# Performance work log

Measured on AMD Instinct MI355X. Metric: run time of the kernel, lower is better.

The kernel has to match this reference:

```python
import jax, jax.numpy as jnp
import numpy as np

EMBED_DIM = 256
NUM_HEADS = 4
HEAD_DIM = EMBED_DIM // NUM_HEADS
SCALE = HEAD_DIM ** (-0.5)


def setup_inputs() -> dict:
    key = jax.random.key(0)
    kx, kq, kp, kb = jax.random.split(key, 4)
    B, N, C = 4, 4096, EMBED_DIM
    x = jax.random.normal(kx, (B, N, C), dtype=jnp.float32)
    # qkv: Linear(C, 3C, bias=False); torch stores weight as [out, in]
    w_qkv = jax.random.normal(kq, (3 * C, C), dtype=jnp.float32) * (C ** -0.5)
    w_proj = jax.random.normal(kp, (C, C), dtype=jnp.float32) * (C ** -0.5)
    b_proj = jax.random.normal(kb, (C,), dtype=jnp.float32) * 0.01
    return {"x": x, "w_qkv": w_qkv, "w_proj": w_proj, "b_proj": b_proj}


def reference(x, w_qkv, w_proj, b_proj):
    B, N, C = x.shape
    H, D = NUM_HEADS, HEAD_DIM
    # qkv projection: [B,N,3C] -> [3,B,H,N,D]
    qkv = (x @ w_qkv.T).reshape(B, N, 3, H, D).transpose(2, 0, 3, 1, 4)
    q, k, v = qkv[0], qkv[1], qkv[2]
    # materialized [B,H,N,N] scores (faithful to the original)
    attn = jnp.einsum("bhnd,bhmd->bhnm", q, k) * SCALE
    attn_probs = jax.nn.softmax(attn, axis=-1)
    out = jnp.einsum("bhnm,bhmd->bhnd", attn_probs, v)
    out = out.transpose(0, 2, 1, 3).reshape(B, N, C)
    return out @ w_proj.T + b_proj
```

## Files before the change

### kernel.cpp

```cpp
#include <hip/hip_runtime.h>
#include <hip/hip_bf16.h>

typedef __hip_bfloat16 bf16;
typedef _Float16 f16;
typedef __attribute__((ext_vector_type(8))) short bf16x8;
typedef __attribute__((ext_vector_type(8))) _Float16 f16x8;
typedef __attribute__((ext_vector_type(2))) _Float16 f16x2;
typedef __attribute__((ext_vector_type(4))) float f32x4;
typedef __attribute__((ext_vector_type(4))) unsigned int u32x4;
typedef __attribute__((ext_vector_type(2))) unsigned int u32x2;

#define B_ 4
#define N_ 4096
#define C_ 256
#define H_ 4
#define D_ 64
#define KLN 0.18033688011112042f

#if __has_builtin(__builtin_amdgcn_exp2f)
#define EXP2(x) __builtin_amdgcn_exp2f(x)
#else
#define EXP2(x) exp2f(x)
#endif
#if __has_builtin(__builtin_amdgcn_rcpf)
#define RCP(x) __builtin_amdgcn_rcpf(x)
#else
#define RCP(x) (1.0f / (x))
#endif

__device__ inline void load_lds16(const void* g, void* l) {
#if __has_builtin(__builtin_amdgcn_global_load_lds)
    __builtin_amdgcn_global_load_lds(
        (const __attribute__((address_space(1))) unsigned int*)g,
        (__attribute__((address_space(3))) unsigned int*)l, 16, 0, 0);
#else
    int ln = __lane_id();
    ((u32x4*)l)[ln] = *((const u32x4*)g);
#endif
}

__device__ inline unsigned int pk2(float a, float b) {
    unsigned int ua = __builtin_bit_cast(unsigned int, a) + 0x8000u;
    unsigned int ub = __builtin_bit_cast(unsigned int, b) + 0x8000u;
    return (ua >> 16) | (ub & 0xffff0000u);
}
__device__ inline unsigned int pkh2(float a, float b) {
#if __has_builtin(__builtin_amdgcn_cvt_pkrtz)
    return __builtin_bit_cast(unsigned int, __builtin_amdgcn_cvt_pkrtz(a, b));
#else
    f16x2 h = { (f16)a, (f16)b };
    return __builtin_bit_cast(unsigned int, h);
#endif
}
__device__ inline short f2s(float x) {
    return (short)__builtin_bit_cast(unsigned short, __float2bfloat16(x));
}
__device__ inline bf16x8 cvt8(const float* __restrict__ p) {
    f32x4 a = *reinterpret_cast<const f32x4*>(p);
    f32x4 b = *reinterpret_cast<const f32x4*>(p + 4);
    bf16x8 r = { f2s(a[0]), f2s(a[1]), f2s(a[2]), f2s(a[3]),
                 f2s(b[0]), f2s(b[1]), f2s(b[2]), f2s(b[3]) };
    return r;
}

__global__ __launch_bounds__(256) void cast_bf16(const float* __restrict__ x,
                                                 const float* __restrict__ wq,
                                                 const float* __restrict__ wp,
                                                 bf16* __restrict__ xb,
                                                 bf16* __restrict__ wqb,
                                                 bf16* __restrict__ wpb)
{
    int bid = blockIdx.x;
    const float* s; bf16* d; int base;
    if (bid < 2048)      { s = x;  d = xb;  base = bid * 2048; }
    else if (bid < 2144) { s = wq; d = wqb; base = (bid - 2048) * 2048; }
    else                 { s = wp; d = wpb; base = (bid - 2144) * 2048; }
    int i = base + threadIdx.x * 8;
    f32x4 a = *reinterpret_cast<const f32x4*>(s + i);
    f32x4 b = *reinterpret_cast<const f32x4*>(s + i + 4);
    u32x4 o;
    o.x = pk2(a[0], a[1]); o.y = pk2(a[2], a[3]);
    o.z = pk2(b[0], b[1]); o.w = pk2(b[2], b[3]);
    *reinterpret_cast<u32x4*>(d + i) = o;
}

__global__ __launch_bounds__(256, 2) void qkv_fast(const bf16* __restrict__ x,
                                                   const bf16* __restrict__ w,
                                                   bf16* __restrict__ qw,
                                                   bf16* __restrict__ kw,
                                                   f16* __restrict__ vtw)
{
    __shared__ short w_s[64][264];
    const int tid  = threadIdx.x;
    const int lane = tid & 63;
    const int wav  = tid >> 6;
    const int quad = lane >> 4;
    const int l16  = lane & 15;
    const int bid = (blockIdx.x & 7) * 192 + (blockIdx.x >> 3);
    const int mt = bid / 12, nb = bid % 12;
    const int m0 = mt * 128, n0 = nb * 64;

    {
        const int row = tid >> 2, cb = (tid & 3) * 64;
        const bf16* src = w + (size_t)(n0 + row) * C_ + cb;
#pragma unroll
        for (int i = 0; i < 8; ++i)
            *reinterpret_cast<bf16x8*>(&w_s[row][cb + i * 8]) =
                *reinterpret_cast<const bf16x8*>(src + i * 8);
    }
    __syncthreads();

#pragma unroll
    for (int half = 0; half < 2; ++half) {
        const int mh = m0 + half * 64;
        f32x4 acc[4] = {{0,0,0,0},{0,0,0,0},{0,0,0,0},{0,0,0,0}};
        const bf16* xrow = x + (size_t)(mh + wav * 16 + l16) * C_ + quad * 8;
        if (nb < 8) {
#pragma unroll
            for (int k0 = 0; k0 < C_; k0 += 32) {
                bf16x8 a = *reinterpret_cast<const bf16x8*>(xrow + k0);
#pragma unroll
                for (int nt = 0; nt < 4; ++nt) {
                    bf16x8 b = *reinterpret_cast<const bf16x8*>(&w_s[nt * 16 + l16][k0 + quad * 8]);
                    acc[nt] = __builtin_amdgcn_mfma_f32_16x16x32_bf16(b, a, acc[nt], 0, 0, 0);
                }
            }
        } else {
#pragma unroll
            for (int k0 = 0; k0 < C_; k0 += 32) {
                bf16x8 a = *reinterpret_cast<const bf16x8*>(xrow + k0);
#pragma unroll
                for (int nt = 0; nt < 4; ++nt) {
                    bf16x8 b = *reinterpret_cast<const bf16x8*>(&w_s[nt * 16 + l16][k0 + quad * 8]);
                    acc[nt] = __builtin_amdgcn_mfma_f32_16x16x32_bf16(a, b, acc[nt], 0, 0, 0);
                }
            }
        }

        const int bb = mh >> 12;
        const int nbase = (mh + wav * 16) & (N_ - 1);
        if (nb < 4) {
            bf16* dst = qw + (((size_t)bb * H_ + nb) * N_ + nbase + l16) * D_;
#pragma unroll
            for (int nt = 0; nt < 4; ++nt) {
                u32x2 wv = { pk2(acc[nt][0] * KLN, acc[nt][1] * KLN),
                             pk2(acc[nt][2] * KLN, acc[nt][3] * KLN) };
                *reinterpret_cast<u32x2*>(dst + nt * 16 + quad * 4) = wv;
            }
        } else if (nb < 8) {
            bf16* dst = kw + (((size_t)bb * H_ + (nb - 4)) * N_ + nbase + l16) * D_;
#pragma unroll
            for (int nt = 0; nt < 4; ++nt) {
                u32x2 wv = { pk2(acc[nt][0], acc[nt][1]),
                             pk2(acc[nt][2], acc[nt][3]) };
                *reinterpret_cast<u32x2*>(dst + nt * 16 + quad * 4) = wv;
            }
        } else {
            const int h = nb - 8;
#pragma unroll
            for (int nt = 0; nt < 4; ++nt) {
                int d = nt * 16 + l16;
                u32x2 wv;
                wv.x = pkh2(acc[nt][0], acc[nt][1]);
                wv.y = pkh2(acc[nt][2], acc[nt][3]);
                *reinterpret_cast<u32x2*>(
                    vtw + (((size_t)bb * H_ + h) * D_ + d) * N_ + nbase + quad * 4) = wv;
            }
        }
    }
}

__global__ __launch_bounds__(256) void qkv_cvt(const float* __restrict__ x,
                                               const float* __restrict__ w,
                                               bf16* __restrict__ qw,
                                               bf16* __restrict__ kw,
                                               f16* __restrict__ vtw)
{
    const int lane = threadIdx.x & 63;
    const int wav  = threadIdx.x >> 6;
    const int quad = lane >> 4;
    const int l16  = lane & 15;
    const int gw   = blockIdx.x * 4 + wav;
    const int m0   = (gw / 12) * 16;
    const int n0   = (gw % 12) * 64;

    f32x4 acc[4] = {{0,0,0,0},{0,0,0,0},{0,0,0,0},{0,0,0,0}};
    const float* xrow = x + (size_t)(m0 + l16) * C_ + quad * 8;
#pragma unroll
    for (int k0 = 0; k0 < C_; k0 += 32) {
        bf16x8 a = cvt8(xrow + k0);
#pragma unroll
        for (int nt = 0; nt < 4; ++nt) {
            bf16x8 b = cvt8(w + (size_t)(n0 + nt * 16 + l16) * C_ + k0 + quad * 8);
            acc[nt] = __builtin_amdgcn_mfma_f32_16x16x32_bf16(a, b, acc[nt], 0, 0, 0);
        }
    }
#pragma unroll
    for (int nt = 0; nt < 4; ++nt)
#pragma unroll
        for (int r = 0; r < 4; ++r) {
            int m  = m0 + quad * 4 + r;
            int o  = n0 + nt * 16 + l16;
            int bb = m >> 12;
            int n  = m & (N_ - 1);
            if (o < 256) {
                int h = o >> 6, d = o & 63;
                qw[(((size_t)bb * H_ + h) * N_ + n) * D_ + d] =
                    __float2bfloat16(acc[nt][r] * KLN);
            } else if (o < 512) {
                int oo = o - 256; int h = oo >> 6, d = oo & 63;
                kw[(((size_t)bb * H_ + h) * N_ + n) * D_ + d] =
                    __float2bfloat16(acc[nt][r]);
            } else {
                int oo = o - 512; int h = oo >> 6, d = oo & 63;
                vtw[(((size_t)bb * H_ + h) * D_ + d) * N_ + n] = (f16)acc[nt][r];
            }
        }
}

__global__ __launch_bounds__(256, 2) void attn(const bf16* __restrict__ q,
                                               const bf16* __restrict__ k,
                                               const f16* __restrict__ vt,
                                               bf16* __restrict__ o)
{
    __shared__ __align__(16) char smem[65536];
    short* k_s = reinterpret_cast<short*>(smem);
    f16*   v_s = reinterpret_cast<f16*>(smem + 32768);

    const int tid  = threadIdx.x;
    const int lane = tid & 63;
    const int wav  = tid >> 6;
    const int quad = lane >> 4;
    const int l16  = lane & 15;
    const int l8   = lane & 7;
    const int sub  = wav & 1;
    const int jh   = wav >> 1;

    const int wg = (blockIdx.x & 7) * 64 + (blockIdx.x >> 3);
    const int bh = wg >> 5;
    const int qt = wg & 31;
    const int bb = bh >> 2, h = bh & 3;

    const bf16* qp = q  + (size_t)bh * N_ * D_;
    const bf16* kp = k  + (size_t)bh * N_ * D_;
    const f16*  vp = vt + (size_t)bh * D_ * N_;

    const int qbase = qt * 128 + sub * 64;
    bf16x8 qb[4][2];
#pragma unroll
    for (int qg = 0; qg < 4; ++qg)
#pragma unroll
        for (int ks = 0; ks < 2; ++ks)
            qb[qg][ks] = *reinterpret_cast<const bf16x8*>(
                qp + (size_t)(qbase + qg * 16 + l16) * D_ + ks * 32 + quad * 8);

    const int ri = lane >> 3;
    const int ci = lane & 7;
    const int gc = ci ^ ri;
    int koff[4], voff[4], lds_r[4];
#pragma unroll
    for (int g = 0; g < 4; ++g) {
        const int rb  = sub * 32 + g * 8;
        const int rho = rb + ri;
        const int pr  = (rho & 32) | ((rho & 12) << 1) | ((rho & 16) >> 2) | (rho & 3);
        koff[g]  = pr * D_ + gc * 8;
        voff[g]  = rho * N_ + gc * 8;
        lds_r[g] = rb * 64;
    }

    f32x4 oacc[4][4];
    f32x4 lv[4];
#pragma unroll
    for (int qg = 0; qg < 4; ++qg) {
        lv[qg] = (f32x4){0, 0, 0, 0};
#pragma unroll
        for (int dt = 0; dt < 4; ++dt) oacc[qg][dt] = (f32x4){0, 0, 0, 0};
    }

    auto stage = [&](int buf, int t) {
        const int j0 = jh * 2048 + t * 64;
        short* kd = k_s + (size_t)(buf * 2 + jh) * 4096;
        f16*   vd = v_s + (size_t)(buf * 2 + jh) * 4096;
#pragma unroll
        for (int g = 0; g < 4; ++g) {
            load_lds16(kp + (size_t)j0 * D_ + koff[g], kd + lds_r[g]);
            load_lds16(vp + j0 + voff[g],              vd + lds_r[g]);
        }
    };

    stage(0, 0);
    __syncthreads();

    for (int t = 0; t < 32; ++t) {
        const int cur = t & 1;
        if (t < 31) stage(cur ^ 1, t + 1);

        const short* kt  = k_s + (size_t)(cur * 2 + jh) * 4096;
        const f16*   vtl = v_s + (size_t)(cur * 2 + jh) * 4096;

        f16x8 pb[4][2];
#pragma unroll
        for (int nt = 0; nt < 4; ++nt) {
            const int rb = (nt * 16 + l16) * 64;
            bf16x8 k0 = *reinterpret_cast<const bf16x8*>(kt + rb + ((quad    ) ^ l8) * 8);
            bf16x8 k1 = *reinterpret_cast<const bf16x8*>(kt + rb + ((4 + quad) ^ l8) * 8);
#pragma unroll
            for (int qg = 0; qg < 4; ++qg) {
                f32x4 sv = __builtin_amdgcn_mfma_f32_16x16x32_bf16(
                    k0, qb[qg][0], (f32x4){0.f, 0.f, 0.f, 0.f}, 0, 0, 0);
                sv = __builtin_amdgcn_mfma_f32_16x16x32_bf16(
                    k1, qb[qg][1], sv, 0, 0, 0);
                f32x4 pa = { EXP2(sv[0]), EXP2(sv[1]), EXP2(sv[2]), EXP2(sv[3]) };
                u32x2 pw = { pkh2(pa[0], pa[1]), pkh2(pa[2], pa[3]) };
                if (nt & 1)
                    *(reinterpret_cast<u32x2*>(&pb[qg][nt >> 1]) + 1) = pw;
                else
                    *(reinterpret_cast<u32x2*>(&pb[qg][nt >> 1]) + 0) = pw;
                lv[qg] += pa;
            }
        }

#pragma unroll
        for (int ks = 0; ks < 2; ++ks)
#pragma unroll
            for (int dt = 0; dt < 4; ++dt) {
                f16x8 va = *reinterpret_cast<const f16x8*>(
                    vtl + (dt * 16 + l16) * 64 + (((ks << 2) + quad) ^ l8) * 8);
#pragma unroll
                for (int qg = 0; qg < 4; ++qg)
                    oacc[qg][dt] = __builtin_amdgcn_mfma_f32_16x16x32_f16(va, pb[qg][ks], oacc[qg][dt], 0, 0, 0);
            }

        __syncthreads();
    }

    float lr[4];
#pragma unroll
    for (int qg = 0; qg < 4; ++qg) {
        float l = (lv[qg][0] + lv[qg][1]) + (lv[qg][2] + lv[qg][3]);
        l += __shfl_xor(l, 16);
        l += __shfl_xor(l, 32);
        lr[qg] = l;
    }

    float* mrg = reinterpret_cast<float*>(smem);
    const int slot = (sub * 64 + lane) * 69;
    if (jh == 1) {
#pragma unroll
        for (int qg = 0; qg < 4; ++qg) {
#pragma unroll
            for (int dt = 0; dt < 4; ++dt)
#pragma unroll
                for (int e = 0; e < 4; ++e)
                    mrg[slot + qg * 17 + dt * 4 + e] = oacc[qg][dt][e];
            mrg[slot + qg * 17 + 16] = lr[qg];
        }
    }
    __syncthreads();
    if (jh == 0) {
#pragma unroll
        for (int qg = 0; qg < 4; ++qg) {
            const float rl = RCP(lr[qg] + mrg[slot + qg * 17 + 16]);
            const size_t obase = ((size_t)bb * N_ + qbase + qg * 16 + l16) * C_ + h * D_;
#pragma unroll
            for (int dt = 0; dt < 4; ++dt) {
                float v0 = (oacc[qg][dt][0] + mrg[slot + qg * 17 + dt * 4 + 0]) * rl;
                float v1 = (oacc[qg][dt][1] + mrg[slot + qg * 17 + dt * 4 + 1]) * rl;
                float v2 = (oacc[qg][dt][2] + mrg[slot + qg * 17 + dt * 4 + 2]) * rl;
                float v3 = (oacc[qg][dt][3] + mrg[slot + qg * 17 + dt * 4 + 3]) * rl;
                u32x2 wv = { pk2(v0, v1), pk2(v2, v3) };
                *reinterpret_cast<u32x2*>(o + obase + dt * 16 + quad * 4) = wv;
            }
        }
    }
}

__global__ __launch_bounds__(256, 2) void out_proj_fast(const bf16* __restrict__ ov,
                                                        const bf16* __restrict__ w,
                                                        const float* __restrict__ bias,
                                                        float* __restrict__ out)
{
    __shared__ short w_s[64][264];
    const int tid  = threadIdx.x;
    const int lane = tid & 63;
    const int wav  = tid >> 6;
    const int quad = lane >> 4;
    const int l16  = lane & 15;
    const int bid = (blockIdx.x & 7) * 64 + (blockIdx.x >> 3);
    const int m0 = (bid >> 2) * 128;
    const int n0 = (bid & 3) * 64;

    {
        const int row = tid >> 2, cb = (tid & 3) * 64;
        const bf16* src = w + (size_t)(n0 + row) * C_ + cb;
#pragma unroll
        for (int i = 0; i < 8; ++i)
            *reinterpret_cast<bf16x8*>(&w_s[row][cb + i * 8]) =
                *reinterpret_cast<const bf16x8*>(src + i * 8);
    }
    __syncthreads();

#pragma unroll
    for (int half = 0; half < 2; ++half) {
        const int mh = m0 + half * 64;
        f32x4 acc[4] = {{0,0,0,0},{0,0,0,0},{0,0,0,0},{0,0,0,0}};
        const bf16* orow = ov + (size_t)(mh + wav * 16 + l16) * C_ + quad * 8;
#pragma unroll
        for (int k0 = 0; k0 < C_; k0 += 32) {
            bf16x8 a = *reinterpret_cast<const bf16x8*>(orow + k0);
#pragma unroll
            for (int nt = 0; nt < 4; ++nt) {
                bf16x8 b = *reinterpret_cast<const bf16x8*>(&w_s[nt * 16 + l16][k0 + quad * 8]);
                acc[nt] = __builtin_amdgcn_mfma_f32_16x16x32_bf16(b, a, acc[nt], 0, 0, 0);
            }
        }
        const int m = mh + wav * 16 + l16;
#pragma unroll
        for (int nt = 0; nt < 4; ++nt) {
            const int oc0 = n0 + nt * 16 + quad * 4;
            f32x4 bv = *reinterpret_cast<const f32x4*>(bias + oc0);
            f32x4 ovv = acc[nt] + bv;
            *reinterpret_cast<f32x4*>(out + (size_t)m * C_ + oc0) = ovv;
        }
    }
}

__global__ __launch_bounds__(256) void out_proj_cvt(const bf16* __restrict__ ov,
                                                    const float* __restrict__ w,
                                                    const float* __restrict__ bias,
                                                    float* __restrict__ out)
{
    const int lane = threadIdx.x & 63;
    const int wav  = threadIdx.x >> 6;
    const int quad = lane >> 4;
    const int l16  = lane & 15;
    const int gw   = blockIdx.x * 4 + wav;
    const int m0   = (gw >> 2) * 16;
    const int n0   = (gw & 3) * 64;

    f32x4 acc[4] = {{0,0,0,0},{0,0,0,0},{0,0,0,0},{0,0,0,0}};
    const bf16* orow = ov + (size_t)(m0 + l16) * C_ + quad * 8;
#pragma unroll
    for (int k0 = 0; k0 < C_; k0 += 32) {
        bf16x8 a = *reinterpret_cast<const bf16x8*>(orow + k0);
#pragma unroll
        for (int nt = 0; nt < 4; ++nt) {
            bf16x8 b = cvt8(w + (size_t)(n0 + nt * 16 + l16) * C_ + k0 + quad * 8);
            acc[nt] = __builtin_amdgcn_mfma_f32_16x16x32_bf16(a, b, acc[nt], 0, 0, 0);
        }
    }
#pragma unroll
    for (int nt = 0; nt < 4; ++nt)
#pragma unroll
        for (int r = 0; r < 4; ++r) {
            int m  = m0 + quad * 4 + r;
            int oc = n0 + nt * 16 + l16;
            out[(size_t)m * C_ + oc] = acc[nt][r] + bias[oc];
        }
}

extern "C" void kernel_launch(void* const* d_in, const int* in_sizes, int n_in,
                              void* d_out, int out_size, void* d_ws, size_t ws_size,
                              hipStream_t stream) {
    const float* x      = (const float*)d_in[0];
    const float* w_qkv  = (const float*)d_in[1];
    const float* w_proj = (const float*)d_in[2];
    const float* b_proj = (const float*)d_in[3];
    float* out = (float*)d_out;

    const size_t qkv_elems = (size_t)B_ * H_ * N_ * D_;
    bf16* q_ws  = (bf16*)d_ws;
    bf16* k_ws  = q_ws  + qkv_elems;
    f16*  vt_ws = (f16*)(k_ws + qkv_elems);
    bf16* o_ws  = (bf16*)(vt_ws + qkv_elems);
    bf16* x_bf  = o_ws  + qkv_elems;
    bf16* wq_bf = x_bf  + (size_t)B_ * N_ * C_;
    bf16* wp_bf = wq_bf + (size_t)3 * C_ * C_;

    const size_t need = ((size_t)4 * qkv_elems + (size_t)B_ * N_ * C_
                         + (size_t)3 * C_ * C_ + (size_t)C_ * C_) * 2;

    if (ws_size >= need) {
        cast_bf16    <<<2176, 256, 0, stream>>>(x, w_qkv, w_proj, x_bf, wq_bf, wp_bf);
        qkv_fast     <<<1536, 256, 0, stream>>>(x_bf, wq_bf, q_ws, k_ws, vt_ws);
        attn         <<< 512, 256, 0, stream>>>(q_ws, k_ws, vt_ws, o_ws);
        out_proj_fast<<< 512, 256, 0, stream>>>(o_ws, wp_bf, b_proj, out);
    } else {
        qkv_cvt      <<<3072, 256, 0, stream>>>(x, w_qkv, q_ws, k_ws, vt_ws);
        attn         <<< 512, 256, 0, stream>>>(q_ws, k_ws, vt_ws, o_ws);
        out_proj_cvt <<<1024, 256, 0, stream>>>(o_ws, w_proj, b_proj, out);
    }
}
```

Baseline: 174.8 us.

## Fuse fp32->bf16 casts into GEMMs and load K/V directly to registers in attention

Removes the separate cast kernel by converting fp32 x and weights to bf16 inside the QKV and output projection kernels. The attention kernel stops staging K/V tiles through LDS with async global-to-LDS copies and a per-tile barrier; each wave now prefetches its K and V fragments straight from global memory into registers for the next tile. This saves a kernel launch and an extra round trip of x through memory, and removes the per-iteration barriers. The cost is more register pressure, and K/V loads are no longer shared across waves, so global/L2 traffic goes up.

```diff
diff --git a/kernel.cpp b/kernel.cpp
--- a/kernel.cpp
+++ b/kernel.cpp
@@ -28,17 +28,6 @@
 #define RCP(x) (1.0f / (x))
 #endif
 
-__device__ inline void load_lds16(const void* g, void* l) {
-#if __has_builtin(__builtin_amdgcn_global_load_lds)
-    __builtin_amdgcn_global_load_lds(
-        (const __attribute__((address_space(1))) unsigned int*)g,
-        (__attribute__((address_space(3))) unsigned int*)l, 16, 0, 0);
-#else
-    int ln = __lane_id();
-    ((u32x4*)l)[ln] = *((const u32x4*)g);
-#endif
-}
-
 __device__ inline unsigned int pk2(float a, float b) {
     unsigned int ua = __builtin_bit_cast(unsigned int, a) + 0x8000u;
     unsigned int ub = __builtin_bit_cast(unsigned int, b) + 0x8000u;
@@ -52,40 +41,16 @@
     return __builtin_bit_cast(unsigned int, h);
 #endif
 }
-__device__ inline short f2s(float x) {
-    return (short)__builtin_bit_cast(unsigned short, __float2bfloat16(x));
-}
-__device__ inline bf16x8 cvt8(const float* __restrict__ p) {
+__device__ inline bf16x8 cvt8pk(const float* __restrict__ p) {
     f32x4 a = *reinterpret_cast<const f32x4*>(p);
     f32x4 b = *reinterpret_cast<const f32x4*>(p + 4);
-    bf16x8 r = { f2s(a[0]), f2s(a[1]), f2s(a[2]), f2s(a[3]),
-                 f2s(b[0]), f2s(b[1]), f2s(b[2]), f2s(b[3]) };
-    return r;
-}
-
-__global__ __launch_bounds__(256) void cast_bf16(const float* __restrict__ x,
-                                                 const float* __restrict__ wq,
-                                                 const float* __restrict__ wp,
-                                                 bf16* __restrict__ xb,
-                                                 bf16* __restrict__ wqb,
-                                                 bf16* __restrict__ wpb)
-{
-    int bid = blockIdx.x;
-    const float* s; bf16* d; int base;
-    if (bid < 2048)      { s = x;  d = xb;  base = bid * 2048; }
-    else if (bid < 2144) { s = wq; d = wqb; base = (bid - 2048) * 2048; }
-    else                 { s = wp; d = wpb; base = (bid - 2144) * 2048; }
-    int i = base + threadIdx.x * 8;
-    f32x4 a = *reinterpret_cast<const f32x4*>(s + i);
-    f32x4 b = *reinterpret_cast<const f32x4*>(s + i + 4);
-    u32x4 o;
-    o.x = pk2(a[0], a[1]); o.y = pk2(a[2], a[3]);
-    o.z = pk2(b[0], b[1]); o.w = pk2(b[2], b[3]);
-    *reinterpret_cast<u32x4*>(d + i) = o;
-}
-
-__global__ __launch_bounds__(256, 2) void qkv_fast(const bf16* __restrict__ x,
-                                                   const bf16* __restrict__ w,
+    u32x4 o = { pk2(a[0], a[1]), pk2(a[2], a[3]),
+                pk2(b[0], b[1]), pk2(b[2], b[3]) };
+    return __builtin_bit_cast(bf16x8, o);
+}
+
+__global__ __launch_bounds__(256, 2) void qkv_fast(const float* __restrict__ x,
+                                                   const float* __restrict__ w,
                                                    bf16* __restrict__ qw,
                                                    bf16* __restrict__ kw,
                                                    f16* __restrict__ vtw)
@@ -102,11 +67,15 @@
 
     {
         const int row = tid >> 2, cb = (tid & 3) * 64;
-        const bf16* src = w + (size_t)(n0 + row) * C_ + cb;
-#pragma unroll
-        for (int i = 0; i < 8; ++i)
-            *reinterpret_cast<bf16x8*>(&w_s[row][cb + i * 8]) =
-                *reinterpret_cast<const bf16x8*>(src + i * 8);
+        const float* src = w + (size_t)(n0 + row) * C_ + cb;
+#pragma unroll
+        for (int i = 0; i < 8; ++i) {
+            f32x4 a = *reinterpret_cast<const f32x4*>(src + i * 8);
+            f32x4 b = *reinterpret_cast<const f32x4*>(src + i * 8 + 4);
+            u32x4 ov = { pk2(a[0], a[1]), pk2(a[2], a[3]),
+                         pk2(b[0], b[1]), pk2(b[2], b[3]) };
+            *reinterpret_cast<u32x4*>(&w_s[row][cb + i * 8]) = ov;
+        }
     }
     __syncthreads();
 
@@ -114,11 +83,11 @@
     for (int half = 0; half < 2; ++half) {
         const int mh = m0 + half * 64;
         f32x4 acc[4] = {{0,0,0,0},{0,0,0,0},{0,0,0,0},{0,0,0,0}};
-        const bf16* xrow = x + (size_t)(mh + wav * 16 + l16) * C_ + quad * 8;
+        const float* xrow = x + (size_t)(mh + wav * 16 + l16) * C_ + quad * 8;
         if (nb < 8) {
 #pragma unroll
             for (int k0 = 0; k0 < C_; k0 += 32) {
-                bf16x8 a = *reinterpret_cast<const bf16x8*>(xrow + k0);
+                bf16x8 a = cvt8pk(xrow + k0);
 #pragma unroll
                 for (int nt = 0; nt < 4; ++nt) {
                     bf16x8 b = *reinterpret_cast<const bf16x8*>(&w_s[nt * 16 + l16][k0 + quad * 8]);
@@ -128,7 +97,7 @@
         } else {
 #pragma unroll
             for (int k0 = 0; k0 < C_; k0 += 32) {
-                bf16x8 a = *reinterpret_cast<const bf16x8*>(xrow + k0);
+                bf16x8 a = cvt8pk(xrow + k0);
 #pragma unroll
                 for (int nt = 0; nt < 4; ++nt) {
                     bf16x8 b = *reinterpret_cast<const bf16x8*>(&w_s[nt * 16 + l16][k0 + quad * 8]);
@@ -170,69 +139,18 @@
     }
 }
 
-__global__ __launch_bounds__(256) void qkv_cvt(const float* __restrict__ x,
-                                               const float* __restrict__ w,
-                                               bf16* __restrict__ qw,
-                                               bf16* __restrict__ kw,
-                                               f16* __restrict__ vtw)
-{
-    const int lane = threadIdx.x & 63;
-    const int wav  = threadIdx.x >> 6;
-    const int quad = lane >> 4;
-    const int l16  = lane & 15;
-    const int gw   = blockIdx.x * 4 + wav;
-    const int m0   = (gw / 12) * 16;
-    const int n0   = (gw % 12) * 64;
-
-    f32x4 acc[4] = {{0,0,0,0},{0,0,0,0},{0,0,0,0},{0,0,0,0}};
-    const float* xrow = x + (size_t)(m0 + l16) * C_ + quad * 8;
-#pragma unroll
-    for (int k0 = 0; k0 < C_; k0 += 32) {
-        bf16x8 a = cvt8(xrow + k0);
-#pragma unroll
-        for (int nt = 0; nt < 4; ++nt) {
-            bf16x8 b = cvt8(w + (size_t)(n0 + nt * 16 + l16) * C_ + k0 + quad * 8);
-            acc[nt] = __builtin_amdgcn_mfma_f32_16x16x32_bf16(a, b, acc[nt], 0, 0, 0);
-        }
-    }
-#pragma unroll
-    for (int nt = 0; nt < 4; ++nt)
-#pragma unroll
-        for (int r = 0; r < 4; ++r) {
-            int m  = m0 + quad * 4 + r;
-            int o  = n0 + nt * 16 + l16;
-            int bb = m >> 12;
-            int n  = m & (N_ - 1);
-            if (o < 256) {
-                int h = o >> 6, d = o & 63;
-                qw[(((size_t)bb * H_ + h) * N_ + n) * D_ + d] =
-                    __float2bfloat16(acc[nt][r] * KLN);
-            } else if (o < 512) {
-                int oo = o - 256; int h = oo >> 6, d = oo & 63;
-                kw[(((size_t)bb * H_ + h) * N_ + n) * D_ + d] =
-                    __float2bfloat16(acc[nt][r]);
-            } else {
-                int oo = o - 512; int h = oo >> 6, d = oo & 63;
-                vtw[(((size_t)bb * H_ + h) * D_ + d) * N_ + n] = (f16)acc[nt][r];
-            }
-        }
-}
-
 __global__ __launch_bounds__(256, 2) void attn(const bf16* __restrict__ q,
                                                const bf16* __restrict__ k,
                                                const f16* __restrict__ vt,
                                                bf16* __restrict__ o)
 {
-    __shared__ __align__(16) char smem[65536];
-    short* k_s = reinterpret_cast<short*>(smem);
-    f16*   v_s = reinterpret_cast<f16*>(smem + 32768);
+    __shared__ float mrg[8832];
 
     const int tid  = threadIdx.x;
     const int lane = tid & 63;
     const int wav  = tid >> 6;
     const int quad = lane >> 4;
     const int l16  = lane & 15;
-    const int l8   = lane & 7;
     const int sub  = wav & 1;
     const int jh   = wav >> 1;
 
@@ -254,18 +172,11 @@
             qb[qg][ks] = *reinterpret_cast<const bf16x8*>(
                 qp + (size_t)(qbase + qg * 16 + l16) * D_ + ks * 32 + quad * 8);
 
-    const int ri = lane >> 3;
-    const int ci = lane & 7;
-    const int gc = ci ^ ri;
-    int koff[4], voff[4], lds_r[4];
-#pragma unroll
-    for (int g = 0; g < 4; ++g) {
-        const int rb  = sub * 32 + g * 8;
-        const int rho = rb + ri;
-        const int pr  = (rho & 32) | ((rho & 12) << 1) | ((rho & 16) >> 2) | (rho & 3);
-        koff[g]  = pr * D_ + gc * 8;
-        voff[g]  = rho * N_ + gc * 8;
-        lds_r[g] = rb * 64;
+    int krow[4];
+#pragma unroll
+    for (int nt = 0; nt < 4; ++nt) {
+        const int rho = nt * 16 + l16;
+        krow[nt] = (rho & 32) | ((rho & 12) << 1) | ((rho & 16) >> 2) | (rho & 3);
     }
 
     f32x4 oacc[4][4];
@@ -277,33 +188,31 @@
         for (int dt = 0; dt < 4; ++dt) oacc[qg][dt] = (f32x4){0, 0, 0, 0};
     }
 
-    auto stage = [&](int buf, int t) {
-        const int j0 = jh * 2048 + t * 64;
-        short* kd = k_s + (size_t)(buf * 2 + jh) * 4096;
-        f16*   vd = v_s + (size_t)(buf * 2 + jh) * 4096;
-#pragma unroll
-        for (int g = 0; g < 4; ++g) {
-            load_lds16(kp + (size_t)j0 * D_ + koff[g], kd + lds_r[g]);
-            load_lds16(vp + j0 + voff[g],              vd + lds_r[g]);
-        }
-    };
-
-    stage(0, 0);
-    __syncthreads();
+    const int j00 = jh * 2048;
+
+    bf16x8 kf[4][2];
+    f16x8  vf[2][4];
+#pragma unroll
+    for (int nt = 0; nt < 4; ++nt)
+#pragma unroll
+        for (int ks = 0; ks < 2; ++ks)
+            kf[nt][ks] = *reinterpret_cast<const bf16x8*>(
+                kp + (size_t)(j00 + krow[nt]) * D_ + ks * 32 + quad * 8);
+#pragma unroll
+    for (int ks = 0; ks < 2; ++ks)
+#pragma unroll
+        for (int dt = 0; dt < 4; ++dt)
+            vf[ks][dt] = *reinterpret_cast<const f16x8*>(
+                vp + (size_t)(dt * 16 + l16) * N_ + j00 + (ks * 4 + quad) * 8);
 
     for (int t = 0; t < 32; ++t) {
-        const int cur = t & 1;
-        if (t < 31) stage(cur ^ 1, t + 1);
-
-        const short* kt  = k_s + (size_t)(cur * 2 + jh) * 4096;
-        const f16*   vtl = v_s + (size_t)(cur * 2 + jh) * 4096;
+        const int jn = j00 + (t + 1) * 64;
 
         f16x8 pb[4][2];
 #pragma unroll
         for (int nt = 0; nt < 4; ++nt) {
-            const int rb = (nt * 16 + l16) * 64;
-            bf16x8 k0 = *reinterpret_cast<const bf16x8*>(kt + rb + ((quad    ) ^ l8) * 8);
-            bf16x8 k1 = *reinterpret_cast<const bf16x8*>(kt + rb + ((4 + quad) ^ l8) * 8);
+            const bf16x8 k0 = kf[nt][0];
+            const bf16x8 k1 = kf[nt][1];
 #pragma unroll
             for (int qg = 0; qg < 4; ++qg) {
                 f32x4 sv = __builtin_amdgcn_mfma_f32_16x16x32_bf16(
@@ -318,20 +227,27 @@
                     *(reinterpret_cast<u32x2*>(&pb[qg][nt >> 1]) + 0) = pw;
                 lv[qg] += pa;
             }
+            if (t < 31) {
+                kf[nt][0] = *reinterpret_cast<const bf16x8*>(
+                    kp + (size_t)(jn + krow[nt]) * D_ + quad * 8);
+                kf[nt][1] = *reinterpret_cast<const bf16x8*>(
+                    kp + (size_t)(jn + krow[nt]) * D_ + 32 + quad * 8);
+            }
         }
 
 #pragma unroll
         for (int ks = 0; ks < 2; ++ks)
 #pragma unroll
             for (int dt = 0; dt < 4; ++dt) {
-                f16x8 va = *reinterpret_cast<const f16x8*>(
-                    vtl + (dt * 16 + l16) * 64 + (((ks << 2) + quad) ^ l8) * 8);
+                const f16x8 va = vf[ks][dt];
 #pragma unroll
                 for (int qg = 0; qg < 4; ++qg)
-                    oacc[qg][dt] = __builtin_amdgcn_mfma_f32_16x16x32_f16(va, pb[qg][ks], oacc[qg][dt], 0, 0, 0);
-            }
-
-        __syncthreads();
+                    oacc[qg][dt] = __builtin_amdgcn_mfma_f32_16x16x32_f16(
+                        va, pb[qg][ks], oacc[qg][dt], 0, 0, 0);
+                if (t < 31)
+                    vf[ks][dt] = *reinterpret_cast<const f16x8*>(
+                        vp + (size_t)(dt * 16 + l16) * N_ + jn + (ks * 4 + quad) * 8);
+            }
     }
 
     float lr[4];
@@ -343,8 +259,8 @@
         lr[qg] = l;
     }
 
-    float* mrg = reinterpret_cast<float*>(smem);
     const int slot = (sub * 64 + lane) * 69;
+    __syncthreads();
     if (jh == 1) {
 #pragma unroll
         for (int qg = 0; qg < 4; ++qg) {
@@ -376,7 +292,7 @@
 }
 
 __global__ __launch_bounds__(256, 2) void out_proj_fast(const bf16* __restrict__ ov,
-                                                        const bf16* __restrict__ w,
+                                                        const float* __restrict__ w,
                                                         const float* __restrict__ bias,
                                                         float* __restrict__ out)
 {
@@ -392,11 +308,15 @@
 
     {
         const int row = tid >> 2, cb = (tid & 3) * 64;
-        const bf16* src = w + (size_t)(n0 + row) * C_ + cb;
-#pragma unroll
-        for (int i = 0; i < 8; ++i)
-            *reinterpret_cast<bf16x8*>(&w_s[row][cb + i * 8]) =
-                *reinterpret_cast<const bf16x8*>(src + i * 8);
+        const float* src = w + (size_t)(n0 + row) * C_ + cb;
+#pragma unroll
+        for (int i = 0; i < 8; ++i) {
+            f32x4 a = *reinterpret_cast<const f32x4*>(src + i * 8);
+            f32x4 b = *reinterpret_cast<const f32x4*>(src + i * 8 + 4);
+            u32x4 ov2 = { pk2(a[0], a[1]), pk2(a[2], a[3]),
+                          pk2(b[0], b[1]), pk2(b[2], b[3]) };
+            *reinterpret_cast<u32x4*>(&w_s[row][cb + i * 8]) = ov2;
+        }
     }
     __syncthreads();
 
@@ -423,40 +343,6 @@
             *reinterpret_cast<f32x4*>(out + (size_t)m * C_ + oc0) = ovv;
         }
     }
-}
-
-__global__ __launch_bounds__(256) void out_proj_cvt(const bf16* __restrict__ ov,
-                                                    const float* __restrict__ w,
-                                                    const float* __restrict__ bias,
-                                                    float* __restrict__ out)
-{
-    const int lane = threadIdx.x & 63;
-    const int wav  = threadIdx.x >> 6;
-    const int quad = lane >> 4;
-    const int l16  = lane & 15;
-    const int gw   = blockIdx.x * 4 + wav;
-    const int m0   = (gw >> 2) * 16;
-    const int n0   = (gw & 3) * 64;
-
-    f32x4 acc[4] = {{0,0,0,0},{0,0,0,0},{0,0,0,0},{0,0,0,0}};
-    const bf16* orow = ov + (size_t)(m0 + l16) * C_ + quad * 8;
-#pragma unroll
-    for (int k0 = 0; k0 < C_; k0 += 32) {
-        bf16x8 a = *reinterpret_cast<const bf16x8*>(orow + k0);
-#pragma unroll
-        for (int nt = 0; nt < 4; ++nt) {
-            bf16x8 b = cvt8(w + (size_t)(n0 + nt * 16 + l16) * C_ + k0 + quad * 8);
-            acc[nt] = __builtin_amdgcn_mfma_f32_16x16x32_bf16(a, b, acc[nt], 0, 0, 0);
-        }
-    }
-#pragma unroll
-    for (int nt = 0; nt < 4; ++nt)
-#pragma unroll
-        for (int r = 0; r < 4; ++r) {
-            int m  = m0 + quad * 4 + r;
-            int oc = n0 + nt * 16 + l16;
-            out[(size_t)m * C_ + oc] = acc[nt][r] + bias[oc];
-        }
 }
 
 extern "C" void kernel_launch(void* const* d_in, const int* in_sizes, int n_in,
@@ -473,21 +359,8 @@
     bf16* k_ws  = q_ws  + qkv_elems;
     f16*  vt_ws = (f16*)(k_ws + qkv_elems);
     bf16* o_ws  = (bf16*)(vt_ws + qkv_elems);
-    bf16* x_bf  = o_ws  + qkv_elems;
-    bf16* wq_bf = x_bf  + (size_t)B_ * N_ * C_;
-    bf16* wp_bf = wq_bf + (size_t)3 * C_ * C_;
-
-    const size_t need = ((size_t)4 * qkv_elems + (size_t)B_ * N_ * C_
-                         + (size_t)3 * C_ * C_ + (size_t)C_ * C_) * 2;
-
-    if (ws_size >= need) {
-        cast_bf16    <<<2176, 256, 0, stream>>>(x, w_qkv, w_proj, x_bf, wq_bf, wp_bf);
-        qkv_fast     <<<1536, 256, 0, stream>>>(x_bf, wq_bf, q_ws, k_ws, vt_ws);
-        attn         <<< 512, 256, 0, stream>>>(q_ws, k_ws, vt_ws, o_ws);
-        out_proj_fast<<< 512, 256, 0, stream>>>(o_ws, wp_bf, b_proj, out);
-    } else {
-        qkv_cvt      <<<3072, 256, 0, stream>>>(x, w_qkv, q_ws, k_ws, vt_ws);
-        attn         <<< 512, 256, 0, stream>>>(q_ws, k_ws, vt_ws, o_ws);
-        out_proj_cvt <<<1024, 256, 0, stream>>>(o_ws, w_proj, b_proj, out);
-    }
-}
+
+    qkv_fast     <<<1536, 256, 0, stream>>>(x, w_qkv, q_ws, k_ws, vt_ws);
+    attn         <<< 512, 256, 0, stream>>>(q_ws, k_ws, vt_ws, o_ws);
+    out_proj_fast<<< 512, 256, 0, stream>>>(o_ws, w_proj, b_proj, out);
+}
```

Result: slower. 241.1 us (+37.9%).
